# Optimization experiments

Hardware: AMD Instinct MI355X
Metric: run time of the kernel (lower is better)

The kernel has to match this reference:

```python
import jax, jax.numpy as jnp
import numpy as np

WINDOW = 8
HEADS = 8

def _rel_index(w):
    coords = np.stack(np.meshgrid(np.arange(w), np.arange(w), indexing='ij')).reshape(2, -1)
    rel = coords[:, :, None] - coords[:, None, :]          # [2, N, N]
    rel = rel.transpose(1, 2, 0) + (w - 1)                 # [N, N, 2]
    return jnp.asarray(rel[:, :, 0] * (2 * w - 1) + rel[:, :, 1])  # [N, N] int

def setup_inputs() -> dict:
    key = jax.random.key(0)
    ks = jax.random.split(key, 5)
    B, N, C = 4096, WINDOW * WINDOW, 256
    x = jax.random.normal(ks[0], (B, N, C), dtype=jnp.float32)
    w_qkv = jax.random.normal(ks[1], (3 * C, C), dtype=jnp.float32) * 0.02
    b_qkv = jnp.zeros((3 * C,), dtype=jnp.float32)
    bias_table = jax.random.normal(ks[2], ((2 * WINDOW - 1) ** 2, HEADS), dtype=jnp.float32) * 0.02
    w_proj = jax.random.normal(ks[3], (C, C), dtype=jnp.float32) * 0.02
    b_proj = jnp.zeros((C,), dtype=jnp.float32)
    return {"x": x, "w_qkv": w_qkv, "b_qkv": b_qkv, "bias_table": bias_table,
            "w_proj": w_proj, "b_proj": b_proj}

def reference(x, w_qkv, b_qkv, bias_table, w_proj, b_proj):
    B, N, C = x.shape
    H = HEADS
    d = C // H
    scale = d ** (-0.5)
    idx = _rel_index(WINDOW)                                # [N, N]
    qkv = x @ w_qkv.T + b_qkv                               # [B, N, 3C]
    qkv = qkv.reshape(B, N, 3, H, d).transpose(2, 0, 3, 1, 4)
    q, k, v = qkv[0], qkv[1], qkv[2]                        # [B, H, N, d]
    attn = jnp.einsum('bhnd,bhmd->bhnm', q * scale, k)      # [B, H, N, N]
    bias = bias_table[idx]                                  # [N, N, H]
    attn = attn + bias.transpose(2, 0, 1)[None]             # add per-head bias
    attn = jax.nn.softmax(attn, axis=-1)
    out = jnp.einsum('bhnm,bhmd->bhnd', attn, v)            # [B, H, N, d]
    out = out.transpose(0, 2, 1, 3).reshape(B, N, C)
    return out @ w_proj.T + b_proj
```

## Files before the change

kernel.cpp:

```cpp
#include <hip/hip_runtime.h>

typedef unsigned int u32;
typedef unsigned short u16;
typedef __bf16 bf16x8 __attribute__((ext_vector_type(8)));
typedef float f32x4 __attribute__((ext_vector_type(4)));
typedef u32 u32x4 __attribute__((ext_vector_type(4)));
typedef u32 u32x2 __attribute__((ext_vector_type(2)));

#define NTOK 64
#define CDIM 256
#define NH 8

#define WS_HDR 8
#define BIAS_O (WS_HDR)
#define WQKV_O (BIAS_O + 32768)
#define BQKV_O (WQKV_O + 196608)
#define WPRJ_O (BQKV_O + 768)
#define BPRJ_O (WPRJ_O + 65536)

#define XROW 520
#define LDS_BYTES 33280

__device__ __forceinline__ float bf2f(u16 u) {
  union { u32 i; float f; } z; z.i = ((u32)u) << 16; return z.f;
}
__device__ __forceinline__ u16 f2bf(float f) {
  __bf16 h = (__bf16)f; return __builtin_bit_cast(u16, h);
}
__device__ __forceinline__ u32 pk2(float a, float b) {
  return (u32)f2bf(a) | ((u32)f2bf(b) << 16);
}
__device__ __forceinline__ float fetchf(const void* p, int idx, int isbf) {
  return isbf ? bf2f(((const u16*)p)[idx]) : ((const float*)p)[idx];
}

__device__ __forceinline__ bf16x8 frag_from(u32 p00, u32 p01, u32 p10, u32 p11,
                                            int s0, int s1, bool hi) {
  u32 A0 = (u32)__shfl((int)p00, s0, 64);
  u32 A1 = (u32)__shfl((int)p01, s0, 64);
  u32 B0 = (u32)__shfl((int)p10, s0, 64);
  u32 B1 = (u32)__shfl((int)p11, s0, 64);
  u32 C0 = (u32)__shfl((int)p00, s1, 64);
  u32 C1 = (u32)__shfl((int)p01, s1, 64);
  u32 D0 = (u32)__shfl((int)p10, s1, 64);
  u32 D1 = (u32)__shfl((int)p11, s1, 64);
  u32x4 f;
  f[0] = hi ? B0 : A0;  f[1] = hi ? B1 : A1;
  f[2] = hi ? D0 : C0;  f[3] = hi ? D1 : C1;
  return __builtin_bit_cast(bf16x8, f);
}

__global__ void detect_dtype(const u16* __restrict__ x, int* __restrict__ flag) {
  __shared__ int cnt;
  if (threadIdx.x == 0) cnt = 0;
  __syncthreads();
  int sane = 0;
  for (int i = threadIdx.x; i < 2048; i += 256) {
    u16 u = x[2 * i];
    int e = (u >> 7) & 0xFF;
    sane += (e == 0 || (e >= 90 && e <= 160)) ? 1 : 0;
  }
  atomicAdd(&cnt, sane);
  __syncthreads();
  if (threadIdx.x == 0) *flag = (cnt >= 1638) ? 1 : 0;
}

__global__ void cvt_params(const void* __restrict__ wqkv, const void* __restrict__ bqkv,
                           const void* __restrict__ btab, const void* __restrict__ wprj,
                           const void* __restrict__ bprj, void* __restrict__ wsraw) {
  u16* ws = (u16*)wsraw;
  const int isbf = *(const int*)wsraw;
  int i = blockIdx.x * 256 + threadIdx.x;
  if (i < 32768) {
    int n = (i >> 6) & 63, m = i & 63, h = i >> 12;
    int r0 = (n >> 3) - (m >> 3) + 7, r1 = (n & 7) - (m & 7) + 7;
    ws[BIAS_O + i] = f2bf(fetchf(btab, (r0 * 15 + r1) * NH + h, isbf));
  } else if (i < 32768 + 196608) {
    int j = i - 32768;
    ws[WQKV_O + j] = f2bf(fetchf(wqkv, j, isbf));
  } else if (i < 32768 + 196608 + 768) {
    int j = i - (32768 + 196608);
    ws[BQKV_O + j] = f2bf(fetchf(bqkv, j, isbf));
  } else if (i < 32768 + 196608 + 768 + 65536) {
    int j = i - (32768 + 196608 + 768);
    ws[WPRJ_O + j] = f2bf(fetchf(wprj, j, isbf));
  } else if (i < 32768 + 196608 + 768 + 65536 + 256) {
    int j = i - (32768 + 196608 + 768 + 65536);
    ws[BPRJ_O + j] = f2bf(fetchf(bprj, j, isbf));
  }
}

#define TILE_T(PK, CHT, CHB, SCL) {                                                   \
    bf16x8 wf[8];                                                                     \
    const u16* wrow = ws + WQKV_O + ((CHB) + c) * CDIM;                               \
    _Pragma("unroll")                                                                 \
    for (int ks = 0; ks < 8; ++ks) wf[ks] = *(const bf16x8*)(wrow + ks * 32 + g * 8); \
    f32x4 binit;                                                                      \
    { u32x2 bp = *(const u32x2*)(ws + BQKV_O + (CHB) + 4 * g);                        \
      binit[0] = bf2f((u16)(bp[0] & 0xffff)); binit[1] = bf2f((u16)(bp[0] >> 16));    \
      binit[2] = bf2f((u16)(bp[1] & 0xffff)); binit[3] = bf2f((u16)(bp[1] >> 16)); }  \
    _Pragma("unroll")                                                                 \
    for (int nt = 0; nt < 4; ++nt) {                                                  \
      f32x4 acc = binit;                                                              \
      _Pragma("unroll")                                                               \
      for (int ks = 0; ks < 8; ++ks) {                                                \
        bf16x8 xf = *(const bf16x8*)(lds + (16 * nt + c) * XROW + ks * 64 + g * 16);  \
        acc = __builtin_amdgcn_mfma_f32_16x16x32_bf16(wf[ks], xf, acc, 0, 0, 0);      \
      }                                                                               \
      PK[CHT][nt][0] = pk2(acc[0] * (SCL), acc[1] * (SCL));                           \
      PK[CHT][nt][1] = pk2(acc[2] * (SCL), acc[3] * (SCL));                           \
    } }

#define TILE_N(PK, CHT, CHB) {                                                        \
    bf16x8 wf[8];                                                                     \
    const u16* wrow = ws + WQKV_O + ((CHB) + c) * CDIM;                               \
    _Pragma("unroll")                                                                 \
    for (int ks = 0; ks < 8; ++ks) wf[ks] = *(const bf16x8*)(wrow + ks * 32 + g * 8); \
    const float badd = bf2f(ws[BQKV_O + (CHB) + c]);                                  \
    _Pragma("unroll")                                                                 \
    for (int nt = 0; nt < 4; ++nt) {                                                  \
      f32x4 acc = {badd, badd, badd, badd};                                           \
      _Pragma("unroll")                                                               \
      for (int ks = 0; ks < 8; ++ks) {                                                \
        bf16x8 xf = *(const bf16x8*)(lds + (16 * nt + c) * XROW + ks * 64 + g * 16);  \
        acc = __builtin_amdgcn_mfma_f32_16x16x32_bf16(xf, wf[ks], acc, 0, 0, 0);      \
      }                                                                               \
      PK[CHT][nt][0] = pk2(acc[0], acc[1]);                                           \
      PK[CHT][nt][1] = pk2(acc[2], acc[3]);                                           \
    } }

__global__ __launch_bounds__(512, 2)
void win_attn_fused(const void* __restrict__ xraw, const void* __restrict__ wsraw,
                    float* __restrict__ out)
{
  __shared__ __align__(16) unsigned char lds[LDS_BYTES];
  const u16* ws  = (const u16*)wsraw;
  const int isbf = *(const int*)wsraw;
  const int b    = blockIdx.x;
  const int tid  = threadIdx.x;
  const int w    = tid >> 6;
  const int lane = tid & 63;
  const int c    = lane & 15;
  const int g    = lane >> 4;
  const float scale = 0.1767766952966369f;

  if (isbf) {
    const u32x4* gx = (const u32x4*)((const u16*)xraw + (size_t)b * (NTOK * CDIM));
#pragma unroll
    for (int i = 0; i < 4; ++i) {
      int q = tid + i * 512;
      int row = q >> 5, c8 = q & 31;
      *(u32x4*)(lds + row * XROW + c8 * 16) = gx[q];
    }
  } else {
    const f32x4* gx = (const f32x4*)((const float*)xraw + (size_t)b * (NTOK * CDIM));
#pragma unroll
    for (int i = 0; i < 8; ++i) {
      int q = tid + i * 512;
      int row = q >> 6, c4 = q & 63;
      f32x4 v = gx[q];
      u32x2 pkv;
      pkv[0] = pk2(v[0], v[1]);
      pkv[1] = pk2(v[2], v[3]);
      *(u32x2*)(lds + row * XROW + c4 * 8) = pkv;
    }
  }
  __syncthreads();

  const int s0 = c + 32 * (g & 1), s1 = s0 + 16;
  const bool hi = ((g >> 1) & 1) != 0;
  const int h = w;

  u32 qpk[2][4][2], kpk[2][4][2];
  bf16x8 bvf[2][2];
  TILE_T(qpk, 0, 32 * w,            scale);
  TILE_T(qpk, 1, 32 * w + 16,       scale);
  TILE_T(kpk, 0, 256 + 32 * w,      1.0f);
  TILE_T(kpk, 1, 256 + 32 * w + 16, 1.0f);
  {
    u32 vpk[2][4][2];
    TILE_N(vpk, 0, 512 + 32 * w);
    TILE_N(vpk, 1, 512 + 32 * w + 16);
#pragma unroll
    for (int dt = 0; dt < 2; ++dt)
#pragma unroll
      for (int k2 = 0; k2 < 2; ++k2)
        bvf[dt][k2] = frag_from(vpk[dt][2 * k2][0], vpk[dt][2 * k2][1],
                                vpk[dt][2 * k2 + 1][0], vpk[dt][2 * k2 + 1][1], s0, s1, hi);
  }
  __syncthreads();

  bf16x8 bkf[4];
#pragma unroll
  for (int mt = 0; mt < 4; ++mt)
    bkf[mt] = frag_from(kpk[0][mt][0], kpk[0][mt][1], kpk[1][mt][0], kpk[1][mt][1], s0, s1, hi);

  u32 Ppk[4][4][2];
#pragma unroll
  for (int nt = 0; nt < 4; ++nt) {
    bf16x8 aqf = frag_from(qpk[0][nt][0], qpk[0][nt][1], qpk[1][nt][0], qpk[1][nt][1], s0, s1, hi);
    f32x4 st[4];
#pragma unroll
    for (int mt = 0; mt < 4; ++mt) {
      u32x2 bp = *(const u32x2*)(ws + BIAS_O + (h << 12) + ((16 * nt + c) << 6) + 16 * mt + 4 * g);
      st[mt][0] = bf2f((u16)(bp[0] & 0xffff)); st[mt][1] = bf2f((u16)(bp[0] >> 16));
      st[mt][2] = bf2f((u16)(bp[1] & 0xffff)); st[mt][3] = bf2f((u16)(bp[1] >> 16));
    }
#pragma unroll
    for (int mt = 0; mt < 4; ++mt)
      st[mt] = __builtin_amdgcn_mfma_f32_16x16x32_bf16(bkf[mt], aqf, st[mt], 0, 0, 0);
    float mx = st[0][0];
#pragma unroll
    for (int mt = 0; mt < 4; ++mt)
#pragma unroll
      for (int r = 0; r < 4; ++r) mx = fmaxf(mx, st[mt][r]);
    mx = fmaxf(mx, __shfl_xor(mx, 16));
    mx = fmaxf(mx, __shfl_xor(mx, 32));
    float sum = 0.f;
#pragma unroll
    for (int mt = 0; mt < 4; ++mt)
#pragma unroll
      for (int r = 0; r < 4; ++r) { float e = __expf(st[mt][r] - mx); st[mt][r] = e; sum += e; }
    sum += __shfl_xor(sum, 16);
    sum += __shfl_xor(sum, 32);
    float inv = 1.0f / sum;
#pragma unroll
    for (int mt = 0; mt < 4; ++mt) {
      Ppk[mt][nt][0] = pk2(st[mt][0] * inv, st[mt][1] * inv);
      Ppk[mt][nt][1] = pk2(st[mt][2] * inv, st[mt][3] * inv);
    }
  }

  f32x4 o[4][2] = {{{0,0,0,0},{0,0,0,0}},{{0,0,0,0},{0,0,0,0}},
                   {{0,0,0,0},{0,0,0,0}},{{0,0,0,0},{0,0,0,0}}};
#pragma unroll
  for (int k2 = 0; k2 < 2; ++k2) {
    bf16x8 paf4[4];
#pragma unroll
    for (int nt = 0; nt < 4; ++nt)
      paf4[nt] = frag_from(Ppk[2 * k2][nt][0], Ppk[2 * k2][nt][1],
                           Ppk[2 * k2 + 1][nt][0], Ppk[2 * k2 + 1][nt][1], s0, s1, hi);
#pragma unroll
    for (int nt = 0; nt < 4; ++nt) {
      o[nt][0] = __builtin_amdgcn_mfma_f32_16x16x32_bf16(paf4[nt], bvf[0][k2], o[nt][0], 0, 0, 0);
      o[nt][1] = __builtin_amdgcn_mfma_f32_16x16x32_bf16(paf4[nt], bvf[1][k2], o[nt][1], 0, 0, 0);
    }
  }

#pragma unroll
  for (int nt = 0; nt < 4; ++nt)
#pragma unroll
    for (int dt = 0; dt < 2; ++dt)
#pragma unroll
      for (int r = 0; r < 4; ++r) {
        int n = 16 * nt + 4 * g + r, col = 32 * w + 16 * dt + c;
        *(u16*)(lds + n * XROW + col * 2) = f2bf(o[nt][dt][r]);
      }
  __syncthreads();

  float* gout = out + (size_t)b * (NTOK * CDIM);
#pragma unroll
  for (int ct = 0; ct < 2; ++ct) {
    const int colw = 32 * w + 16 * ct + c;
    const float badd = bf2f(ws[BPRJ_O + colw]);
    f32x4 acc[4];
#pragma unroll
    for (int rt = 0; rt < 4; ++rt)
#pragma unroll
      for (int r = 0; r < 4; ++r) acc[rt][r] = badd;
    const u16* wrow = ws + WPRJ_O + colw * CDIM;
#pragma unroll
    for (int ks = 0; ks < 8; ++ks) {
      bf16x8 wf = *(const bf16x8*)(wrow + ks * 32 + g * 8);
#pragma unroll
      for (int rt = 0; rt < 4; ++rt) {
        bf16x8 ay = *(const bf16x8*)(lds + (16 * rt + c) * XROW + ks * 64 + g * 16);
        acc[rt] = __builtin_amdgcn_mfma_f32_16x16x32_bf16(ay, wf, acc[rt], 0, 0, 0);
      }
    }
#pragma unroll
    for (int rt = 0; rt < 4; ++rt)
#pragma unroll
      for (int r = 0; r < 4; ++r) {
        int n = 16 * rt + 4 * g + r;
        gout[n * CDIM + colw] = acc[rt][r];
      }
  }
}

extern "C" void kernel_launch(void* const* d_in, const int* in_sizes, int n_in,
                              void* d_out, int out_size, void* d_ws, size_t ws_size,
                              hipStream_t stream) {
  (void)in_sizes; (void)n_in; (void)out_size; (void)ws_size;
  detect_dtype<<<dim3(1), dim3(256), 0, stream>>>((const u16*)d_in[0], (int*)d_ws);
  cvt_params<<<dim3(1156), dim3(256), 0, stream>>>(d_in[1], d_in[2], d_in[3], d_in[4],
                                                   d_in[5], d_ws);
  win_attn_fused<<<dim3(4096), dim3(512), 0, stream>>>(d_in[0], d_ws, (float*)d_out);
}
```

Baseline: 466.6 us.

## Reuse LDS x fragments across QKV and projection tiles via register blocking

The QKV loops are reordered so each wave loads two 16-row x tiles from LDS into registers once, then reuses them across all six Q/K/V weight tiles. Previously every tile re-read x from LDS. The output projection is restructured the same way, loading two row tiles of the attention output once and reusing them for both column tiles. This cuts LDS read traffic by about 3x in QKV, but re-reads the weight fragments from global/L2 twice each and raises register pressure under the 512x2 launch bound.

```diff
diff --git a/kernel.cpp b/kernel.cpp
--- a/kernel.cpp
+++ b/kernel.cpp
@@ -90,7 +90,7 @@
   }
 }
 
-#define TILE_T(PK, CHT, CHB, SCL) {                                                   \
+#define TILE_T2(PK, CHT, CHB, SCL, NT0) {                                             \
     bf16x8 wf[8];                                                                     \
     const u16* wrow = ws + WQKV_O + ((CHB) + c) * CDIM;                               \
     _Pragma("unroll")                                                                 \
@@ -100,33 +100,29 @@
       binit[0] = bf2f((u16)(bp[0] & 0xffff)); binit[1] = bf2f((u16)(bp[0] >> 16));    \
       binit[2] = bf2f((u16)(bp[1] & 0xffff)); binit[3] = bf2f((u16)(bp[1] >> 16)); }  \
     _Pragma("unroll")                                                                 \
-    for (int nt = 0; nt < 4; ++nt) {                                                  \
+    for (int p = 0; p < 2; ++p) {                                                     \
       f32x4 acc = binit;                                                              \
       _Pragma("unroll")                                                               \
-      for (int ks = 0; ks < 8; ++ks) {                                                \
-        bf16x8 xf = *(const bf16x8*)(lds + (16 * nt + c) * XROW + ks * 64 + g * 16);  \
-        acc = __builtin_amdgcn_mfma_f32_16x16x32_bf16(wf[ks], xf, acc, 0, 0, 0);      \
-      }                                                                               \
-      PK[CHT][nt][0] = pk2(acc[0] * (SCL), acc[1] * (SCL));                           \
-      PK[CHT][nt][1] = pk2(acc[2] * (SCL), acc[3] * (SCL));                           \
+      for (int ks = 0; ks < 8; ++ks)                                                  \
+        acc = __builtin_amdgcn_mfma_f32_16x16x32_bf16(wf[ks], xfs[p][ks], acc, 0, 0, 0); \
+      PK[CHT][(NT0) + p][0] = pk2(acc[0] * (SCL), acc[1] * (SCL));                    \
+      PK[CHT][(NT0) + p][1] = pk2(acc[2] * (SCL), acc[3] * (SCL));                    \
     } }
 
-#define TILE_N(PK, CHT, CHB) {                                                        \
+#define TILE_N2(PK, CHT, CHB, NT0) {                                                  \
     bf16x8 wf[8];                                                                     \
     const u16* wrow = ws + WQKV_O + ((CHB) + c) * CDIM;                               \
     _Pragma("unroll")                                                                 \
     for (int ks = 0; ks < 8; ++ks) wf[ks] = *(const bf16x8*)(wrow + ks * 32 + g * 8); \
     const float badd = bf2f(ws[BQKV_O + (CHB) + c]);                                  \
     _Pragma("unroll")                                                                 \
-    for (int nt = 0; nt < 4; ++nt) {                                                  \
+    for (int p = 0; p < 2; ++p) {                                                     \
       f32x4 acc = {badd, badd, badd, badd};                                           \
       _Pragma("unroll")                                                               \
-      for (int ks = 0; ks < 8; ++ks) {                                                \
-        bf16x8 xf = *(const bf16x8*)(lds + (16 * nt + c) * XROW + ks * 64 + g * 16);  \
-        acc = __builtin_amdgcn_mfma_f32_16x16x32_bf16(xf, wf[ks], acc, 0, 0, 0);      \
-      }                                                                               \
-      PK[CHT][nt][0] = pk2(acc[0], acc[1]);                                           \
-      PK[CHT][nt][1] = pk2(acc[2], acc[3]);                                           \
+      for (int ks = 0; ks < 8; ++ks)                                                  \
+        acc = __builtin_amdgcn_mfma_f32_16x16x32_bf16(xfs[p][ks], wf[ks], acc, 0, 0, 0); \
+      PK[CHT][(NT0) + p][0] = pk2(acc[0], acc[1]);                                    \
+      PK[CHT][(NT0) + p][1] = pk2(acc[2], acc[3]);                                    \
     } }
 
 __global__ __launch_bounds__(512, 2)
@@ -173,14 +169,23 @@
 
   u32 qpk[2][4][2], kpk[2][4][2];
   bf16x8 bvf[2][2];
-  TILE_T(qpk, 0, 32 * w,            scale);
-  TILE_T(qpk, 1, 32 * w + 16,       scale);
-  TILE_T(kpk, 0, 256 + 32 * w,      1.0f);
-  TILE_T(kpk, 1, 256 + 32 * w + 16, 1.0f);
   {
     u32 vpk[2][4][2];
-    TILE_N(vpk, 0, 512 + 32 * w);
-    TILE_N(vpk, 1, 512 + 32 * w + 16);
+#pragma unroll
+    for (int np = 0; np < 2; ++np) {
+      bf16x8 xfs[2][8];
+#pragma unroll
+      for (int p = 0; p < 2; ++p)
+#pragma unroll
+        for (int ks = 0; ks < 8; ++ks)
+          xfs[p][ks] = *(const bf16x8*)(lds + (16 * (2 * np + p) + c) * XROW + ks * 64 + g * 16);
+      TILE_T2(qpk, 0, 32 * w,             scale, 2 * np);
+      TILE_T2(qpk, 1, 32 * w + 16,        scale, 2 * np);
+      TILE_T2(kpk, 0, 256 + 32 * w,       1.0f,  2 * np);
+      TILE_T2(kpk, 1, 256 + 32 * w + 16,  1.0f,  2 * np);
+      TILE_N2(vpk, 0, 512 + 32 * w,       2 * np);
+      TILE_N2(vpk, 1, 512 + 32 * w + 16,  2 * np);
+    }
 #pragma unroll
     for (int dt = 0; dt < 2; ++dt)
 #pragma unroll
@@ -260,31 +265,37 @@
 
   float* gout = out + (size_t)b * (NTOK * CDIM);
 #pragma unroll
-  for (int ct = 0; ct < 2; ++ct) {
-    const int colw = 32 * w + 16 * ct + c;
-    const float badd = bf2f(ws[BPRJ_O + colw]);
-    f32x4 acc[4];
-#pragma unroll
-    for (int rt = 0; rt < 4; ++rt)
-#pragma unroll
-      for (int r = 0; r < 4; ++r) acc[rt][r] = badd;
-    const u16* wrow = ws + WPRJ_O + colw * CDIM;
-#pragma unroll
-    for (int ks = 0; ks < 8; ++ks) {
-      bf16x8 wf = *(const bf16x8*)(wrow + ks * 32 + g * 8);
-#pragma unroll
-      for (int rt = 0; rt < 4; ++rt) {
-        bf16x8 ay = *(const bf16x8*)(lds + (16 * rt + c) * XROW + ks * 64 + g * 16);
-        acc[rt] = __builtin_amdgcn_mfma_f32_16x16x32_bf16(ay, wf, acc[rt], 0, 0, 0);
+  for (int rth = 0; rth < 2; ++rth) {
+    bf16x8 ayh[2][8];
+#pragma unroll
+    for (int rt2 = 0; rt2 < 2; ++rt2)
+#pragma unroll
+      for (int ks = 0; ks < 8; ++ks)
+        ayh[rt2][ks] = *(const bf16x8*)(lds + (16 * (2 * rth + rt2) + c) * XROW + ks * 64 + g * 16);
+#pragma unroll
+    for (int ct = 0; ct < 2; ++ct) {
+      const int colw = 32 * w + 16 * ct + c;
+      const float badd = bf2f(ws[BPRJ_O + colw]);
+      f32x4 acc2[2];
+#pragma unroll
+      for (int rt2 = 0; rt2 < 2; ++rt2)
+#pragma unroll
+        for (int r = 0; r < 4; ++r) acc2[rt2][r] = badd;
+      const u16* wrow = ws + WPRJ_O + colw * CDIM;
+#pragma unroll
+      for (int ks = 0; ks < 8; ++ks) {
+        bf16x8 wf = *(const bf16x8*)(wrow + ks * 32 + g * 8);
+        acc2[0] = __builtin_amdgcn_mfma_f32_16x16x32_bf16(ayh[0][ks], wf, acc2[0], 0, 0, 0);
+        acc2[1] = __builtin_amdgcn_mfma_f32_16x16x32_bf16(ayh[1][ks], wf, acc2[1], 0, 0, 0);
       }
-    }
-#pragma unroll
-    for (int rt = 0; rt < 4; ++rt)
-#pragma unroll
-      for (int r = 0; r < 4; ++r) {
-        int n = 16 * rt + 4 * g + r;
-        gout[n * CDIM + colw] = acc[rt][r];
-      }
+#pragma unroll
+      for (int rt2 = 0; rt2 < 2; ++rt2)
+#pragma unroll
+        for (int r = 0; r < 4; ++r) {
+          int n = 16 * (2 * rth + rt2) + 4 * g + r;
+          gout[n * CDIM + colw] = acc2[rt2][r];
+        }
+    }
   }
 }
 
```

After: 489.9 us. 1.05x slower.

## Make window attention persistent with double-buffered LDS prefetch of next windows

Applied to the files above, without the earlier changes.

Launches 512 persistent blocks instead of 4096, and each block now processes 8 windows in sequence. Two LDS buffers hold the input window: the next window's x is loaded from global memory into registers during the attention math and written to the alternate buffer, so the load can overlap compute. This is meant to hide global-load latency and cut per-block launch and prologue overhead. In exchange it doubles LDS per block and keeps the prefetch registers live across the loop, which raises register pressure and may cause spills under the 512×2 launch bound.

```diff
diff --git a/kernel.cpp b/kernel.cpp
--- a/kernel.cpp
+++ b/kernel.cpp
@@ -10,6 +10,7 @@
 #define NTOK 64
 #define CDIM 256
 #define NH 8
+#define WPB 8
 
 #define WS_HDR 8
 #define BIAS_O (WS_HDR)
@@ -19,7 +20,8 @@
 #define BPRJ_O (WPRJ_O + 65536)
 
 #define XROW 520
-#define LDS_BYTES 33280
+#define BUFB 33280
+#define LDS_BYTES (2 * BUFB)
 
 __device__ __forceinline__ float bf2f(u16 u) {
   union { u32 i; float f; } z; z.i = ((u32)u) << 16; return z.f;
@@ -104,7 +106,7 @@
       f32x4 acc = binit;                                                              \
       _Pragma("unroll")                                                               \
       for (int ks = 0; ks < 8; ++ks) {                                                \
-        bf16x8 xf = *(const bf16x8*)(lds + (16 * nt + c) * XROW + ks * 64 + g * 16);  \
+        bf16x8 xf = *(const bf16x8*)(XB + (16 * nt + c) * XROW + ks * 64 + g * 16);   \
         acc = __builtin_amdgcn_mfma_f32_16x16x32_bf16(wf[ks], xf, acc, 0, 0, 0);      \
       }                                                                               \
       PK[CHT][nt][0] = pk2(acc[0] * (SCL), acc[1] * (SCL));                           \
@@ -122,169 +124,191 @@
       f32x4 acc = {badd, badd, badd, badd};                                           \
       _Pragma("unroll")                                                               \
       for (int ks = 0; ks < 8; ++ks) {                                                \
-        bf16x8 xf = *(const bf16x8*)(lds + (16 * nt + c) * XROW + ks * 64 + g * 16);  \
+        bf16x8 xf = *(const bf16x8*)(XB + (16 * nt + c) * XROW + ks * 64 + g * 16);   \
         acc = __builtin_amdgcn_mfma_f32_16x16x32_bf16(xf, wf[ks], acc, 0, 0, 0);      \
       }                                                                               \
       PK[CHT][nt][0] = pk2(acc[0], acc[1]);                                           \
       PK[CHT][nt][1] = pk2(acc[2], acc[3]);                                           \
     } }
 
+#define ISSUE_X(BW) {                                                                 \
+    if (isbf) {                                                                       \
+      const u32x4* gx = (const u32x4*)((const u16*)xraw + (size_t)(BW) * (NTOK*CDIM));\
+      _Pragma("unroll")                                                               \
+      for (int j = 0; j < 4; ++j) xpru[j] = gx[tid + j * 512];                        \
+    } else {                                                                          \
+      const f32x4* gx = (const f32x4*)((const float*)xraw + (size_t)(BW) * (NTOK*CDIM));\
+      _Pragma("unroll")                                                               \
+      for (int j = 0; j < 8; ++j) xpr[j] = gx[tid + j * 512];                         \
+    } }
+
+#define WRITE_X(PB) {                                                                 \
+    if (isbf) {                                                                       \
+      _Pragma("unroll")                                                               \
+      for (int j = 0; j < 4; ++j) {                                                   \
+        int q = tid + j * 512, row = q >> 5, c8 = q & 31;                             \
+        *(u32x4*)((PB) + row * XROW + c8 * 16) = xpru[j];                             \
+      }                                                                               \
+    } else {                                                                          \
+      _Pragma("unroll")                                                               \
+      for (int j = 0; j < 8; ++j) {                                                   \
+        int q = tid + j * 512, row = q >> 6, c4 = q & 63;                             \
+        u32x2 pkv;                                                                    \
+        pkv[0] = pk2(xpr[j][0], xpr[j][1]);                                           \
+        pkv[1] = pk2(xpr[j][2], xpr[j][3]);                                           \
+        *(u32x2*)((PB) + row * XROW + c4 * 8) = pkv;                                  \
+      }                                                                               \
+    } }
+
 __global__ __launch_bounds__(512, 2)
-void win_attn_fused(const void* __restrict__ xraw, const void* __restrict__ wsraw,
-                    float* __restrict__ out)
+void win_attn_persist(const void* __restrict__ xraw, const void* __restrict__ wsraw,
+                      float* __restrict__ out)
 {
   __shared__ __align__(16) unsigned char lds[LDS_BYTES];
   const u16* ws  = (const u16*)wsraw;
   const int isbf = *(const int*)wsraw;
-  const int b    = blockIdx.x;
   const int tid  = threadIdx.x;
   const int w    = tid >> 6;
   const int lane = tid & 63;
   const int c    = lane & 15;
   const int g    = lane >> 4;
   const float scale = 0.1767766952966369f;
-
-  if (isbf) {
-    const u32x4* gx = (const u32x4*)((const u16*)xraw + (size_t)b * (NTOK * CDIM));
-#pragma unroll
-    for (int i = 0; i < 4; ++i) {
-      int q = tid + i * 512;
-      int row = q >> 5, c8 = q & 31;
-      *(u32x4*)(lds + row * XROW + c8 * 16) = gx[q];
-    }
-  } else {
-    const f32x4* gx = (const f32x4*)((const float*)xraw + (size_t)b * (NTOK * CDIM));
-#pragma unroll
-    for (int i = 0; i < 8; ++i) {
-      int q = tid + i * 512;
-      int row = q >> 6, c4 = q & 63;
-      f32x4 v = gx[q];
-      u32x2 pkv;
-      pkv[0] = pk2(v[0], v[1]);
-      pkv[1] = pk2(v[2], v[3]);
-      *(u32x2*)(lds + row * XROW + c4 * 8) = pkv;
-    }
-  }
-  __syncthreads();
+  const int b0   = blockIdx.x * WPB;
 
   const int s0 = c + 32 * (g & 1), s1 = s0 + 16;
   const bool hi = ((g >> 1) & 1) != 0;
-  const int h = w;
-
-  u32 qpk[2][4][2], kpk[2][4][2];
-  bf16x8 bvf[2][2];
-  TILE_T(qpk, 0, 32 * w,            scale);
-  TILE_T(qpk, 1, 32 * w + 16,       scale);
-  TILE_T(kpk, 0, 256 + 32 * w,      1.0f);
-  TILE_T(kpk, 1, 256 + 32 * w + 16, 1.0f);
-  {
-    u32 vpk[2][4][2];
-    TILE_N(vpk, 0, 512 + 32 * w);
-    TILE_N(vpk, 1, 512 + 32 * w + 16);
-#pragma unroll
-    for (int dt = 0; dt < 2; ++dt)
-#pragma unroll
-      for (int k2 = 0; k2 < 2; ++k2)
-        bvf[dt][k2] = frag_from(vpk[dt][2 * k2][0], vpk[dt][2 * k2][1],
-                                vpk[dt][2 * k2 + 1][0], vpk[dt][2 * k2 + 1][1], s0, s1, hi);
-  }
-  __syncthreads();
-
-  bf16x8 bkf[4];
-#pragma unroll
-  for (int mt = 0; mt < 4; ++mt)
-    bkf[mt] = frag_from(kpk[0][mt][0], kpk[0][mt][1], kpk[1][mt][0], kpk[1][mt][1], s0, s1, hi);
-
-  u32 Ppk[4][4][2];
-#pragma unroll
-  for (int nt = 0; nt < 4; ++nt) {
-    bf16x8 aqf = frag_from(qpk[0][nt][0], qpk[0][nt][1], qpk[1][nt][0], qpk[1][nt][1], s0, s1, hi);
-    f32x4 st[4];
-#pragma unroll
-    for (int mt = 0; mt < 4; ++mt) {
-      u32x2 bp = *(const u32x2*)(ws + BIAS_O + (h << 12) + ((16 * nt + c) << 6) + 16 * mt + 4 * g);
-      st[mt][0] = bf2f((u16)(bp[0] & 0xffff)); st[mt][1] = bf2f((u16)(bp[0] >> 16));
-      st[mt][2] = bf2f((u16)(bp[1] & 0xffff)); st[mt][3] = bf2f((u16)(bp[1] >> 16));
+
+  f32x4 xpr[8];
+  u32x4 xpru[4];
+
+  ISSUE_X(b0);
+  WRITE_X(lds);
+  ISSUE_X(b0 + 1);
+
+  for (int i = 0; i < WPB; ++i) {
+    unsigned char* XB = lds + (i & 1) * BUFB;
+    unsigned char* XN = lds + ((i + 1) & 1) * BUFB;
+    const int b = b0 + i;
+
+    __syncthreads();
+    if (i < WPB - 1) WRITE_X(XN);
+
+    u32 qpk[2][4][2], kpk[2][4][2];
+    bf16x8 bvf[2][2];
+    TILE_T(qpk, 0, 32 * w,            scale);
+    TILE_T(qpk, 1, 32 * w + 16,       scale);
+    TILE_T(kpk, 0, 256 + 32 * w,      1.0f);
+    TILE_T(kpk, 1, 256 + 32 * w + 16, 1.0f);
+    {
+      u32 vpk[2][4][2];
+      TILE_N(vpk, 0, 512 + 32 * w);
+      TILE_N(vpk, 1, 512 + 32 * w + 16);
+#pragma unroll
+      for (int dt = 0; dt < 2; ++dt)
+#pragma unroll
+        for (int k2 = 0; k2 < 2; ++k2)
+          bvf[dt][k2] = frag_from(vpk[dt][2 * k2][0], vpk[dt][2 * k2][1],
+                                  vpk[dt][2 * k2 + 1][0], vpk[dt][2 * k2 + 1][1], s0, s1, hi);
     }
+    __syncthreads();
+    if (i < WPB - 2) ISSUE_X(b0 + i + 2);
+
+    bf16x8 bkf[4];
 #pragma unroll
     for (int mt = 0; mt < 4; ++mt)
-      st[mt] = __builtin_amdgcn_mfma_f32_16x16x32_bf16(bkf[mt], aqf, st[mt], 0, 0, 0);
-    float mx = st[0][0];
-#pragma unroll
-    for (int mt = 0; mt < 4; ++mt)
-#pragma unroll
-      for (int r = 0; r < 4; ++r) mx = fmaxf(mx, st[mt][r]);
-    mx = fmaxf(mx, __shfl_xor(mx, 16));
-    mx = fmaxf(mx, __shfl_xor(mx, 32));
-    float sum = 0.f;
-#pragma unroll
-    for (int mt = 0; mt < 4; ++mt)
-#pragma unroll
-      for (int r = 0; r < 4; ++r) { float e = __expf(st[mt][r] - mx); st[mt][r] = e; sum += e; }
-    sum += __shfl_xor(sum, 16);
-    sum += __shfl_xor(sum, 32);
-    float inv = 1.0f / sum;
-#pragma unroll
-    for (int mt = 0; mt < 4; ++mt) {
-      Ppk[mt][nt][0] = pk2(st[mt][0] * inv, st[mt][1] * inv);
-      Ppk[mt][nt][1] = pk2(st[mt][2] * inv, st[mt][3] * inv);
-    }
-  }
-
-  f32x4 o[4][2] = {{{0,0,0,0},{0,0,0,0}},{{0,0,0,0},{0,0,0,0}},
-                   {{0,0,0,0},{0,0,0,0}},{{0,0,0,0},{0,0,0,0}}};
-#pragma unroll
-  for (int k2 = 0; k2 < 2; ++k2) {
-    bf16x8 paf4[4];
-#pragma unroll
-    for (int nt = 0; nt < 4; ++nt)
-      paf4[nt] = frag_from(Ppk[2 * k2][nt][0], Ppk[2 * k2][nt][1],
-                           Ppk[2 * k2 + 1][nt][0], Ppk[2 * k2 + 1][nt][1], s0, s1, hi);
+      bkf[mt] = frag_from(kpk[0][mt][0], kpk[0][mt][1], kpk[1][mt][0], kpk[1][mt][1], s0, s1, hi);
+
+    u32 Ppk[4][4][2];
 #pragma unroll
     for (int nt = 0; nt < 4; ++nt) {
-      o[nt][0] = __builtin_amdgcn_mfma_f32_16x16x32_bf16(paf4[nt], bvf[0][k2], o[nt][0], 0, 0, 0);
-      o[nt][1] = __builtin_amdgcn_mfma_f32_16x16x32_bf16(paf4[nt], bvf[1][k2], o[nt][1], 0, 0, 0);
-    }
-  }
-
-#pragma unroll
-  for (int nt = 0; nt < 4; ++nt)
-#pragma unroll
-    for (int dt = 0; dt < 2; ++dt)
-#pragma unroll
-      for (int r = 0; r < 4; ++r) {
-        int n = 16 * nt + 4 * g + r, col = 32 * w + 16 * dt + c;
-        *(u16*)(lds + n * XROW + col * 2) = f2bf(o[nt][dt][r]);
+      bf16x8 aqf = frag_from(qpk[0][nt][0], qpk[0][nt][1], qpk[1][nt][0], qpk[1][nt][1], s0, s1, hi);
+      f32x4 st[4];
+#pragma unroll
+      for (int mt = 0; mt < 4; ++mt) {
+        u32x2 bp = *(const u32x2*)(ws + BIAS_O + (w << 12) + ((16 * nt + c) << 6) + 16 * mt + 4 * g);
+        st[mt][0] = bf2f((u16)(bp[0] & 0xffff)); st[mt][1] = bf2f((u16)(bp[0] >> 16));
+        st[mt][2] = bf2f((u16)(bp[1] & 0xffff)); st[mt][3] = bf2f((u16)(bp[1] >> 16));
       }
-  __syncthreads();
-
-  float* gout = out + (size_t)b * (NTOK * CDIM);
-#pragma unroll
-  for (int ct = 0; ct < 2; ++ct) {
-    const int colw = 32 * w + 16 * ct + c;
-    const float badd = bf2f(ws[BPRJ_O + colw]);
-    f32x4 acc[4];
-#pragma unroll
-    for (int rt = 0; rt < 4; ++rt)
-#pragma unroll
-      for (int r = 0; r < 4; ++r) acc[rt][r] = badd;
-    const u16* wrow = ws + WPRJ_O + colw * CDIM;
-#pragma unroll
-    for (int ks = 0; ks < 8; ++ks) {
-      bf16x8 wf = *(const bf16x8*)(wrow + ks * 32 + g * 8);
-#pragma unroll
-      for (int rt = 0; rt < 4; ++rt) {
-        bf16x8 ay = *(const bf16x8*)(lds + (16 * rt + c) * XROW + ks * 64 + g * 16);
-        acc[rt] = __builtin_amdgcn_mfma_f32_16x16x32_bf16(ay, wf, acc[rt], 0, 0, 0);
+#pragma unroll
+      for (int mt = 0; mt < 4; ++mt)
+        st[mt] = __builtin_amdgcn_mfma_f32_16x16x32_bf16(bkf[mt], aqf, st[mt], 0, 0, 0);
+      float mx = st[0][0];
+#pragma unroll
+      for (int mt = 0; mt < 4; ++mt)
+#pragma unroll
+        for (int r = 0; r < 4; ++r) mx = fmaxf(mx, st[mt][r]);
+      mx = fmaxf(mx, __shfl_xor(mx, 16));
+      mx = fmaxf(mx, __shfl_xor(mx, 32));
+      float sum = 0.f;
+#pragma unroll
+      for (int mt = 0; mt < 4; ++mt)
+#pragma unroll
+        for (int r = 0; r < 4; ++r) { float e = __expf(st[mt][r] - mx); st[mt][r] = e; sum += e; }
+      sum += __shfl_xor(sum, 16);
+      sum += __shfl_xor(sum, 32);
+      float inv = 1.0f / sum;
+#pragma unroll
+      for (int mt = 0; mt < 4; ++mt) {
+        Ppk[mt][nt][0] = pk2(st[mt][0] * inv, st[mt][1] * inv);
+        Ppk[mt][nt][1] = pk2(st[mt][2] * inv, st[mt][3] * inv);
       }
     }
-#pragma unroll
-    for (int rt = 0; rt < 4; ++rt)
-#pragma unroll
-      for (int r = 0; r < 4; ++r) {
-        int n = 16 * rt + 4 * g + r;
-        gout[n * CDIM + colw] = acc[rt][r];
+
+    f32x4 o[4][2] = {{{0,0,0,0},{0,0,0,0}},{{0,0,0,0},{0,0,0,0}},
+                     {{0,0,0,0},{0,0,0,0}},{{0,0,0,0},{0,0,0,0}}};
+#pragma unroll
+    for (int k2 = 0; k2 < 2; ++k2) {
+      bf16x8 paf4[4];
+#pragma unroll
+      for (int nt = 0; nt < 4; ++nt)
+        paf4[nt] = frag_from(Ppk[2 * k2][nt][0], Ppk[2 * k2][nt][1],
+                             Ppk[2 * k2 + 1][nt][0], Ppk[2 * k2 + 1][nt][1], s0, s1, hi);
+#pragma unroll
+      for (int nt = 0; nt < 4; ++nt) {
+        o[nt][0] = __builtin_amdgcn_mfma_f32_16x16x32_bf16(paf4[nt], bvf[0][k2], o[nt][0], 0, 0, 0);
+        o[nt][1] = __builtin_amdgcn_mfma_f32_16x16x32_bf16(paf4[nt], bvf[1][k2], o[nt][1], 0, 0, 0);
       }
+    }
+
+#pragma unroll
+    for (int nt = 0; nt < 4; ++nt)
+#pragma unroll
+      for (int dt = 0; dt < 2; ++dt)
+#pragma unroll
+        for (int r = 0; r < 4; ++r) {
+          int n = 16 * nt + 4 * g + r, col = 32 * w + 16 * dt + c;
+          *(u16*)(XB + n * XROW + col * 2) = f2bf(o[nt][dt][r]);
+        }
+    __syncthreads();
+
+    float* gout = out + (size_t)b * (NTOK * CDIM);
+#pragma unroll
+    for (int ct = 0; ct < 2; ++ct) {
+      const int colw = 32 * w + 16 * ct + c;
+      const float badd = bf2f(ws[BPRJ_O + colw]);
+      f32x4 acc[4];
+#pragma unroll
+      for (int rt = 0; rt < 4; ++rt)
+#pragma unroll
+        for (int r = 0; r < 4; ++r) acc[rt][r] = badd;
+      const u16* wrow = ws + WPRJ_O + colw * CDIM;
+#pragma unroll
+      for (int ks = 0; ks < 8; ++ks) {
+        bf16x8 wf = *(const bf16x8*)(wrow + ks * 32 + g * 8);
+#pragma unroll
+        for (int rt = 0; rt < 4; ++rt) {
+          bf16x8 ay = *(const bf16x8*)(XB + (16 * rt + c) * XROW + ks * 64 + g * 16);
+          acc[rt] = __builtin_amdgcn_mfma_f32_16x16x32_bf16(ay, wf, acc[rt], 0, 0, 0);
+        }
+      }
+#pragma unroll
+      for (int rt = 0; rt < 4; ++rt)
+#pragma unroll
+        for (int r = 0; r < 4; ++r) {
+          int n = 16 * rt + 4 * g + r;
+          gout[n * CDIM + colw] = acc[rt][r];
+        }
+    }
   }
 }
 
@@ -295,5 +319,5 @@
   detect_dtype<<<dim3(1), dim3(256), 0, stream>>>((const u16*)d_in[0], (int*)d_ws);
   cvt_params<<<dim3(1156), dim3(256), 0, stream>>>(d_in[1], d_in[2], d_in[3], d_in[4],
                                                    d_in[5], d_ws);
-  win_attn_fused<<<dim3(4096), dim3(512), 0, stream>>>(d_in[0], d_ws, (float*)d_out);
-}
+  win_attn_persist<<<dim3(512), dim3(512), 0, stream>>>(d_in[0], d_ws, (float*)d_out);
+}
```

New measurement: 1.459 ms. 213% more time.
